# Kernel optimization log

Measured on AMD Instinct MI355X. Metric: run time of the kernel, lower is better.

The kernel has to match this reference:

```python
import jax, jax.numpy as jnp
import numpy as np
import math


def _sinusoidal_pe(T, C, base=10000.0, dtype=jnp.float32):
    # Vaswani et al. interleaved sin/cos positional encoding, shape (T, C)
    position = jnp.arange(T, dtype=jnp.float32)[:, None]                      # (T,1)
    div_term = jnp.exp(jnp.arange(0, C, 2, dtype=jnp.float32) * (-math.log(base) / C))  # (C/2,)
    pe = jnp.zeros((T, C), dtype=jnp.float32)
    pe = pe.at[:, 0::2].set(jnp.sin(position * div_term))
    pe = pe.at[:, 1::2].set(jnp.cos(position * div_term))
    return pe.astype(dtype)


def setup_inputs() -> dict:
    key = jax.random.key(0)
    ks = jax.random.split(key, 7)
    B, T, C = 16, 8192, 1024
    s = 1.0 / math.sqrt(C)
    return {
        "x":   jax.random.normal(ks[0], (B, T, C), dtype=jnp.float32),
        "Wq":  jax.random.normal(ks[1], (C, C), dtype=jnp.float32) * s,
        "bq":  jax.random.normal(ks[2], (C,), dtype=jnp.float32) * s,
        "Wkv": jax.random.normal(ks[3], (C, 2 * C), dtype=jnp.float32) * s,
        "bkv": jax.random.normal(ks[4], (2 * C,), dtype=jnp.float32) * s,
        "Wo":  jax.random.normal(ks[5], (C, C), dtype=jnp.float32) * s,
        "bo":  jax.random.normal(ks[6], (C,), dtype=jnp.float32) * s,
    }


def reference(x, Wq, bq, Wkv, bkv, Wo, bo):
    B, T, C = x.shape
    H = 16
    D = C // H  # head_dim = 64

    # sinusoidal positional encoding (scale=False -> just add)
    x = x + _sinusoidal_pe(T, C, dtype=x.dtype)[None]

    # single-query projection (first token only) + full K/V projection
    q = x[:, :1, :] @ Wq + bq                       # (B, 1, C)
    kv = x @ Wkv + bkv                              # (B, T, 2C)
    k, v = kv[..., :C], kv[..., C:]                 # (B, T, C)

    # split heads
    q = q.reshape(B, 1, H, D).transpose(0, 2, 1, 3)  # (B, H, 1, D)
    k = k.reshape(B, T, H, D).transpose(0, 2, 1, 3)  # (B, H, T, D)
    v = v.reshape(B, T, H, D).transpose(0, 2, 1, 3)  # (B, H, T, D)

    # decode-style SDPA: one query vs T keys
    scale = 1.0 / math.sqrt(D)
    scores = jnp.einsum('bhqd,bhkd->bhqk', q, k) * scale   # (B, H, 1, T)
    attn = jax.nn.softmax(scores, axis=-1)
    y = jnp.einsum('bhqk,bhkd->bhqd', attn, v)             # (B, H, 1, D)

    # merge heads -> (B, C) and output projection
    y = y.transpose(0, 2, 1, 3).reshape(B, C)
    return y @ Wo + bo
```

## Files before the change

kernel.cpp:

```cpp
#include <hip/hip_runtime.h>
#include <math.h>

#define B 16
#define T 8192
#define C 1024
#define H 16
#define D 64

#define NCHUNK 32
#define CHUNK  256
#define RS     16
#define NST    (CHUNK/RS)

typedef unsigned short ushort_t;
typedef unsigned int uint_t;

typedef _Float16 half8  __attribute__((ext_vector_type(8)));
typedef _Float16 half4v __attribute__((ext_vector_type(4)));
typedef float    float4v __attribute__((ext_vector_type(4)));


__global__ void k_fdiv(double* __restrict__ fdiv) {
    int c = blockIdx.x * 256 + threadIdx.x;
    if (c < C) {
        int i2 = c & ~1;
        double e = exp((double)i2 * (-9.210340371976184 / 1024.0));
        fdiv[c] = e * 0.15915494309189535;
    }
}

__global__ void __launch_bounds__(256) k_q(const float* __restrict__ x,
                                           const float* __restrict__ Wq,
                                           const float* __restrict__ bq,
                                           float* __restrict__ q) {
    __shared__ float xst[C][4];
    __shared__ float red[4][64][4];
    int cblk = blockIdx.x >> 2, bg = blockIdx.x & 3;
    for (int i = threadIdx.x; i < 4 * C; i += 256) {
        int b4 = i >> 10, k = i & 1023;
        xst[k][b4] = x[(size_t)(bg * 4 + b4) * T * C + k] + ((k & 1) ? 1.0f : 0.0f);
    }
    __syncthreads();
    int col = threadIdx.x & 63;
    int kg  = threadIdx.x >> 6;
    int c = cblk * 64 + col;
    float a[4] = {0.f, 0.f, 0.f, 0.f};
#pragma unroll 4
    for (int k = kg * 256; k < kg * 256 + 256; ++k) {
        float w = Wq[(size_t)k * C + c];
        float4v xv = *(const float4v*)&xst[k][0];
#pragma unroll
        for (int j = 0; j < 4; ++j) a[j] += xv[j] * w;
    }
#pragma unroll
    for (int j = 0; j < 4; ++j) red[kg][col][j] = a[j];
    __syncthreads();
    if (kg == 0) {
#pragma unroll
        for (int j = 0; j < 4; ++j)
            q[(size_t)(bg * 4 + j) * C + c] =
                bq[c] + red[0][col][j] + red[1][col][j] + red[2][col][j] + red[3][col][j];
    }
}

__global__ void __launch_bounds__(256) k_rt(const float* __restrict__ Wkv,
                                            const float* __restrict__ bkv,
                                            const float* __restrict__ q,
                                            float* __restrict__ rt,
                                            float* __restrict__ cc) {
    __shared__ float qs[16][64];
    int h = blockIdx.x >> 2, cq = blockIdx.x & 3;
    for (int i = threadIdx.x; i < 16 * 64; i += 256) {
        int b = i >> 6, d = i & 63;
        qs[b][d] = q[(size_t)b * C + h * 64 + d];
    }
    __syncthreads();
    int c = cq * 256 + threadIdx.x;
    const float4* wrow = (const float4*)(Wkv + (size_t)c * (2 * C) + h * 64);
    float acc[16];
#pragma unroll
    for (int b = 0; b < 16; ++b) acc[b] = 0.f;
#pragma unroll
    for (int d4 = 0; d4 < 16; ++d4) {
        float4 w = wrow[d4];
#pragma unroll
        for (int b = 0; b < 16; ++b) {
            const float4* q4 = (const float4*)&qs[b][d4 * 4];
            acc[b] += w.x * q4->x + w.y * q4->y + w.z * q4->z + w.w * q4->w;
        }
    }
#pragma unroll
    for (int b = 0; b < 16; ++b)
        rt[((size_t)b * C + c) * H + h] = acc[b] * 0.125f;
    if (cq == 0 && threadIdx.x < 16) {
        int b = threadIdx.x;
        float a = 0.f;
        for (int d = 0; d < 64; ++d) a += bkv[h * 64 + d] * qs[b][d];
        cc[b * H + h] = a * 0.125f;
    }
}

__global__ void __launch_bounds__(256, 2)
k_fused(const float* __restrict__ x,
        const float* __restrict__ rt,
        const float* __restrict__ cc,
        const double* __restrict__ fdiv,
        float* __restrict__ pacc,
        float* __restrict__ pl) {
    __shared__ _Float16 xa[2][RS * 1024];
    __shared__ float Sred[4 * RS * 16];
    __shared__ float p_lds[RS * 16];
    __shared__ float l_lds[16];
    __shared__ float cc_sh[16];

    const int tid = threadIdx.x;
    const int b  = blockIdx.x >> 5;
    const int t0 = (blockIdx.x & 31) * CHUNK;
    const int lane = tid & 63;
    const int wv   = tid >> 6;
    const int c0   = tid * 4;

    if (tid < 16) { cc_sh[tid] = cc[b * H + tid]; l_lds[tid] = 0.f; }

    const int m = lane & 15, g = lane >> 4;
    half8 rhf[8], rlf[8];
#pragma unroll
    for (int ks = 0; ks < 8; ++ks) {
#pragma unroll
        for (int j = 0; j < 8; ++j) {
            int c = wv * 256 + ks * 32 + g * 8 + j;
            float v = rt[((size_t)b * C + c) * H + m];
            _Float16 hi = (_Float16)v;
            rhf[ks][j] = hi;
            rlf[ks][j] = (_Float16)(v - (float)hi);
        }
    }

    const double fd0 = fdiv[c0];
    const double fd1 = fdiv[c0 + 2];
    const float* xbase = x + ((size_t)b * T + t0) * C + c0;

    float4v acc[16];
#pragma unroll
    for (int h = 0; h < 16; ++h) acc[h] = (float4v){0.f, 0.f, 0.f, 0.f};

    float4v xr[16];

    auto loadregs = [&](int st) {
        const float* xs = xbase + (size_t)st * RS * C;
#pragma unroll
        for (int r = 0; r < RS; ++r)
            xr[r] = *(const float4v*)(xs + (size_t)r * C);
    };
    auto pewrite = [&](int st, int buf) {
#pragma unroll
        for (int r = 0; r < RS; ++r) {
            double td = (double)(t0 + st * RS + r);
            double rev0 = td * fd0;
            double rev1 = td * fd1;
            float a0 = (float)(rev0 - floor(rev0)) * 6.283185307179586f;
            float a1 = (float)(rev1 - floor(rev1)) * 6.283185307179586f;
            float sn0, cs0, sn1, cs1;
            __sincosf(a0, &sn0, &cs0);
            __sincosf(a1, &sn1, &cs1);
            half4v hv;
            hv[0] = (_Float16)(xr[r][0] + sn0);
            hv[1] = (_Float16)(xr[r][1] + cs0);
            hv[2] = (_Float16)(xr[r][2] + sn1);
            hv[3] = (_Float16)(xr[r][3] + cs1);
            int elem = (r * 1024 + c0) ^ ((r & 7) << 3);
            *(half4v*)&xa[buf][elem] = hv;
        }
    };

    loadregs(0);
    pewrite(0, 0);
    __syncthreads();

    for (int st = 0; st < NST; ++st) {
        const int cur = st & 1;
        if (st + 1 < NST) loadregs(st + 1);

        float4v sac = {0.f, 0.f, 0.f, 0.f};
        const int abase = m * 1024 + wv * 256 + g * 8;
        const int aswz  = (m & 7) << 3;
#pragma unroll
        for (int ks = 0; ks < 8; ++ks) {
            half8 af = *(const half8*)&xa[cur][(abase + ks * 32) ^ aswz];
            sac = __builtin_amdgcn_mfma_f32_16x16x32_f16(af, rhf[ks], sac, 0, 0, 0);
            sac = __builtin_amdgcn_mfma_f32_16x16x32_f16(af, rlf[ks], sac, 0, 0, 0);
        }
#pragma unroll
        for (int rg = 0; rg < 4; ++rg)
            Sred[wv * 256 + (g * 4 + rg) * 16 + m] = sac[rg];

        if (st + 1 < NST) pewrite(st + 1, cur ^ 1);
        __syncthreads();

        {
            float s = Sred[tid] + Sred[256 + tid] + Sred[512 + tid] + Sred[768 + tid]
                    + cc_sh[tid & 15];
            p_lds[tid] = __expf(s);
        }
        __syncthreads();

        if (tid < 16) {
            float ls = 0.f;
#pragma unroll
            for (int r = 0; r < RS; ++r) ls += p_lds[r * 16 + tid];
            l_lds[tid] += ls;
        }
#pragma unroll 2
        for (int r = 0; r < RS; ++r) {
            int elem = (r * 1024 + c0) ^ ((r & 7) << 3);
            half4v xv = *(const half4v*)&xa[cur][elem];
            float4v xvf = {(float)xv[0], (float)xv[1], (float)xv[2], (float)xv[3]};
            const float4v* pr = (const float4v*)&p_lds[r * 16];
            float4v p0 = pr[0], p1 = pr[1], p2 = pr[2], p3 = pr[3];
            float pvv[16] = {p0[0], p0[1], p0[2], p0[3],
                             p1[0], p1[1], p1[2], p1[3],
                             p2[0], p2[1], p2[2], p2[3],
                             p3[0], p3[1], p3[2], p3[3]};
#pragma unroll
            for (int h = 0; h < 16; ++h)
                acc[h] += xvf * pvv[h];
        }
        __syncthreads();
    }

    float* pb = pacc + (size_t)blockIdx.x * (H * C) + c0;
#pragma unroll
    for (int h = 0; h < 16; ++h)
        *(float4v*)&pb[h * 1024] = acc[h];
    if (tid < 16) pl[blockIdx.x * 16 + tid] = l_lds[tid];
}

__global__ void __launch_bounds__(256) k_y(const float* __restrict__ Wkv,
                                           const float* __restrict__ bkv,
                                           const float* __restrict__ pacc,
                                           const float* __restrict__ pl,
                                           float* __restrict__ y) {
    __shared__ float st_[C][4];
    __shared__ float red[4][64][4];
    __shared__ float invl[4];
    int h = blockIdx.x >> 2, bg = blockIdx.x & 3;
    int c0 = threadIdx.x * 4;
#pragma unroll
    for (int b4 = 0; b4 < 4; ++b4) {
        int b = bg * 4 + b4;
        float4v s = {0.f, 0.f, 0.f, 0.f};
#pragma unroll 4
        for (int ch = 0; ch < NCHUNK; ++ch)
            s += *(const float4v*)&pacc[(((size_t)b * NCHUNK + ch) * H + h) * 1024 + c0];
        st_[c0 + 0][b4] = s[0];
        st_[c0 + 1][b4] = s[1];
        st_[c0 + 2][b4] = s[2];
        st_[c0 + 3][b4] = s[3];
    }
    if (threadIdx.x < 4) {
        int b = bg * 4 + threadIdx.x;
        float l = 0.f;
#pragma unroll
        for (int ch = 0; ch < NCHUNK; ++ch) l += pl[(b * NCHUNK + ch) * H + h];
        invl[threadIdx.x] = 1.0f / l;
    }
    __syncthreads();
    int col = threadIdx.x & 63, kg = threadIdx.x >> 6;
    int cy = h * 64 + col;
    float a[4] = {0.f, 0.f, 0.f, 0.f};
#pragma unroll 4
    for (int c = kg * 256; c < kg * 256 + 256; ++c) {
        float w = Wkv[(size_t)c * (2 * C) + C + cy];
        float4v sv = *(const float4v*)&st_[c][0];
#pragma unroll
        for (int j = 0; j < 4; ++j) a[j] += sv[j] * w;
    }
#pragma unroll
    for (int j = 0; j < 4; ++j) red[kg][col][j] = a[j];
    __syncthreads();
    if (kg == 0) {
#pragma unroll
        for (int j = 0; j < 4; ++j)
            y[(size_t)(bg * 4 + j) * C + cy] =
                bkv[C + cy] +
                (red[0][col][j] + red[1][col][j] + red[2][col][j] + red[3][col][j]) * invl[j];
    }
}

__global__ void __launch_bounds__(256) k_out(const float* __restrict__ Wo,
                                             const float* __restrict__ bo,
                                             const float* __restrict__ y,
                                             float* __restrict__ out) {
    __shared__ float yt[C][4];
    __shared__ float red[4][64][4];
    int jb = blockIdx.x >> 2, bg = blockIdx.x & 3;
    for (int i = threadIdx.x; i < 4 * C; i += 256) {
        int b4 = i >> 10, k = i & 1023;
        yt[k][b4] = y[(size_t)(bg * 4 + b4) * C + k];
    }
    __syncthreads();
    int col = threadIdx.x & 63, kg = threadIdx.x >> 6;
    int j = jb * 64 + col;
    float a[4] = {0.f, 0.f, 0.f, 0.f};
#pragma unroll 4
    for (int k = kg * 256; k < kg * 256 + 256; ++k) {
        float w = Wo[(size_t)k * C + j];
        float4v yv = *(const float4v*)&yt[k][0];
#pragma unroll
        for (int jj = 0; jj < 4; ++jj) a[jj] += yv[jj] * w;
    }
#pragma unroll
    for (int jj = 0; jj < 4; ++jj) red[kg][col][jj] = a[jj];
    __syncthreads();
    if (kg == 0) {
#pragma unroll
        for (int jj = 0; jj < 4; ++jj)
            out[(size_t)(bg * 4 + jj) * C + j] =
                bo[j] + red[0][col][jj] + red[1][col][jj] + red[2][col][jj] + red[3][col][jj];
    }
}

extern "C" void kernel_launch(void* const* d_in, const int* in_sizes, int n_in,
                              void* d_out, int out_size, void* d_ws, size_t ws_size,
                              hipStream_t stream) {
    const float* x   = (const float*)d_in[0];
    const float* Wq  = (const float*)d_in[1];
    const float* bq  = (const float*)d_in[2];
    const float* Wkv = (const float*)d_in[3];
    const float* bkv = (const float*)d_in[4];
    const float* Wo  = (const float*)d_in[5];
    const float* bo  = (const float*)d_in[6];
    float* out = (float*)d_out;

    char* w = (char*)d_ws;
    double* fdiv = (double*)w;
    float* q     = (float*)(w + 8192);
    float* rt    = q + (size_t)B * C;
    float* cc    = rt + (size_t)B * C * H;
    float* y     = cc + B * H;
    float* pacc  = y + B * C;
    float* pl    = pacc + (size_t)(B * NCHUNK) * H * C;

    k_fdiv<<<4, 256, 0, stream>>>(fdiv);
    k_q<<<64, 256, 0, stream>>>(x, Wq, bq, q);
    k_rt<<<64, 256, 0, stream>>>(Wkv, bkv, q, rt, cc);
    k_fused<<<B * NCHUNK, 256, 0, stream>>>(x, rt, cc, fdiv, pacc, pl);
    k_y<<<64, 256, 0, stream>>>(Wkv, bkv, pacc, pl, y);
    k_out<<<64, 256, 0, stream>>>(Wo, bo, y, out);
}
```

Measured before the change: 843.2 us.

## Drop register-prefetch double buffering in favor of single LDS buffer staging

```diff
diff --git a/kernel.cpp b/kernel.cpp
--- a/kernel.cpp
+++ b/kernel.cpp
@@ -107,7 +107,7 @@
         const double* __restrict__ fdiv,
         float* __restrict__ pacc,
         float* __restrict__ pl) {
-    __shared__ _Float16 xa[2][RS * 1024];
+    __shared__ _Float16 xa[RS * 1024];
     __shared__ float Sred[4 * RS * 16];
     __shared__ float p_lds[RS * 16];
     __shared__ float l_lds[16];
@@ -138,23 +138,18 @@
 
     const double fd0 = fdiv[c0];
     const double fd1 = fdiv[c0 + 2];
+
     const float* xbase = x + ((size_t)b * T + t0) * C + c0;
 
     float4v acc[16];
 #pragma unroll
     for (int h = 0; h < 16; ++h) acc[h] = (float4v){0.f, 0.f, 0.f, 0.f};
 
-    float4v xr[16];
-
-    auto loadregs = [&](int st) {
+    auto stage = [&](int st) {
         const float* xs = xbase + (size_t)st * RS * C;
-#pragma unroll
-        for (int r = 0; r < RS; ++r)
-            xr[r] = *(const float4v*)(xs + (size_t)r * C);
-    };
-    auto pewrite = [&](int st, int buf) {
-#pragma unroll
+#pragma unroll 4
         for (int r = 0; r < RS; ++r) {
+            float4v xv = *(const float4v*)(xs + (size_t)r * C);
             double td = (double)(t0 + st * RS + r);
             double rev0 = td * fd0;
             double rev1 = td * fd1;
@@ -164,37 +159,31 @@
             __sincosf(a0, &sn0, &cs0);
             __sincosf(a1, &sn1, &cs1);
             half4v hv;
-            hv[0] = (_Float16)(xr[r][0] + sn0);
-            hv[1] = (_Float16)(xr[r][1] + cs0);
-            hv[2] = (_Float16)(xr[r][2] + sn1);
-            hv[3] = (_Float16)(xr[r][3] + cs1);
+            hv[0] = (_Float16)(xv[0] + sn0);
+            hv[1] = (_Float16)(xv[1] + cs0);
+            hv[2] = (_Float16)(xv[2] + sn1);
+            hv[3] = (_Float16)(xv[3] + cs1);
             int elem = (r * 1024 + c0) ^ ((r & 7) << 3);
-            *(half4v*)&xa[buf][elem] = hv;
+            *(half4v*)&xa[elem] = hv;
         }
     };
 
-    loadregs(0);
-    pewrite(0, 0);
+    stage(0);
     __syncthreads();
 
     for (int st = 0; st < NST; ++st) {
-        const int cur = st & 1;
-        if (st + 1 < NST) loadregs(st + 1);
-
         float4v sac = {0.f, 0.f, 0.f, 0.f};
         const int abase = m * 1024 + wv * 256 + g * 8;
         const int aswz  = (m & 7) << 3;
 #pragma unroll
         for (int ks = 0; ks < 8; ++ks) {
-            half8 af = *(const half8*)&xa[cur][(abase + ks * 32) ^ aswz];
+            half8 af = *(const half8*)&xa[(abase + ks * 32) ^ aswz];
             sac = __builtin_amdgcn_mfma_f32_16x16x32_f16(af, rhf[ks], sac, 0, 0, 0);
             sac = __builtin_amdgcn_mfma_f32_16x16x32_f16(af, rlf[ks], sac, 0, 0, 0);
         }
 #pragma unroll
         for (int rg = 0; rg < 4; ++rg)
             Sred[wv * 256 + (g * 4 + rg) * 16 + m] = sac[rg];
-
-        if (st + 1 < NST) pewrite(st + 1, cur ^ 1);
         __syncthreads();
 
         {
@@ -213,7 +202,7 @@
 #pragma unroll 2
         for (int r = 0; r < RS; ++r) {
             int elem = (r * 1024 + c0) ^ ((r & 7) << 3);
-            half4v xv = *(const half4v*)&xa[cur][elem];
+            half4v xv = *(const half4v*)&xa[elem];
             float4v xvf = {(float)xv[0], (float)xv[1], (float)xv[2], (float)xv[3]};
             const float4v* pr = (const float4v*)&p_lds[r * 16];
             float4v p0 = pr[0], p1 = pr[1], p2 = pr[2], p3 = pr[3];
@@ -225,6 +214,8 @@
             for (int h = 0; h < 16; ++h)
                 acc[h] += xvf * pvv[h];
         }
+        __syncthreads();
+        if (st + 1 < NST) stage(st + 1);
         __syncthreads();
     }
 
```

Result: no change. 829.9 us (-1.6%).
